# Kernel optimization log

Measured on AMD Instinct MI355X. Metric: run time of the kernel, lower is better.

Reference implementation:

```python
import jax, jax.numpy as jnp
import numpy as np

PRIMES = (2, 3, 5, 7, 11, 13, 17, 19, 23, 29)
TEMP = 1000.0  # softmax_temperature
B, S = 32, 2048

def _templates(p):
    # circle template for residue r: (cos(2*pi*r/p), sin(2*pi*r/p)) -> [p, 2]
    ang = 2.0 * np.pi * np.arange(p) / p
    return jnp.asarray(np.stack([np.cos(ang), np.sin(ang)], axis=-1).astype(np.float32))

def _mul_onehot(p):
    # onehot[a, b, (a*b) % p] = 1 -> [p, p, p]
    t = (np.arange(p)[:, None] * np.arange(p)[None, :]) % p
    return jnp.asarray((t[..., None] == np.arange(p)).astype(np.float32))

TEMPLATES = [_templates(p) for p in PRIMES]
MUL_OH = [_mul_onehot(p) for p in PRIMES]

def setup_inputs() -> dict:
    key = jax.random.key(0)
    k1, k2 = jax.random.split(key)
    m = len(PRIMES)
    return {
        "a_circle": jax.random.normal(k1, (B, S, m, 2), dtype=jnp.float32),
        "b_circle": jax.random.normal(k2, (B, S, m, 2), dtype=jnp.float32),
    }

def _circle_add(a, b):
    # complex multiply: angles add -> (a + b) mod p on the circle
    ca, sa = a[..., 0], a[..., 1]
    cb, sb = b[..., 0], b[..., 1]
    return jnp.stack([ca * cb - sa * sb, sa * cb + ca * sb], axis=-1)

def _circle_sub(a, b):
    # a - b = a + conj(b): negate sin of b
    b_conj = jnp.stack([b[..., 0], -b[..., 1]], axis=-1)
    return _circle_add(a, b_conj)

def _decode_soft(c_i, tmpl):
    # c_i: [B, S, 2], tmpl: [p, 2] -> soft one-hot over residues [B, S, p]
    sim = jnp.einsum('bsd,pd->bsp', c_i, tmpl)
    return jax.nn.softmax(TEMP * sim, axis=-1)

def _circle_mul(a, b):
    outs = []
    for i, p in enumerate(PRIMES):
        tmpl = TEMPLATES[i]
        a_soft = _decode_soft(a[:, :, i, :], tmpl)
        b_soft = _decode_soft(b[:, :, i, :], tmpl)
        # outer product of soft residues contracted with mul table
        dist = jnp.einsum('bsi,bsj,ijk->bsk', a_soft, b_soft, MUL_OH[i])
        outs.append(dist @ tmpl)  # re-encode to circle: [B, S, 2]
    return jnp.stack(outs, axis=2)  # [B, S, m, 2]

def reference(a_circle, b_circle):
    add = _circle_add(a_circle, b_circle)
    sub = _circle_sub(a_circle, b_circle)
    mul = _circle_mul(a_circle, b_circle)
    return jnp.stack([add, sub, mul], axis=0)  # [3, B, S, m, 2]
```

## Files before the change

### kernel.cpp

```cpp
#include <hip/hip_runtime.h>


#define SOFTMAX_TEMP 1000.0f

constexpr double PI_D = 3.14159265358979323846264338327950288;

constexpr double tay_cos(double x) {
    double x2 = x * x, term = 1.0, sum = 1.0;
    for (int k = 1; k <= 15; ++k) { term *= -x2 / double((2 * k - 1) * (2 * k)); sum += term; }
    return sum;
}
constexpr double tay_sin(double x) {
    double x2 = x * x, term = x, sum = x;
    for (int k = 1; k <= 15; ++k) { term *= -x2 / double((2 * k) * (2 * k + 1)); sum += term; }
    return sum;
}

template <int P> struct Tab { float c[P]; float s[P]; };

template <int P>
constexpr Tab<P> make_tab() {
    Tab<P> t{};
    for (int r = 0; r < P; ++r) {
        double x = 2.0 * PI_D * double(r) / double(P);
        if (x > PI_D) x -= 2.0 * PI_D;
        t.c[r] = (float)tay_cos(x);
        t.s[r] = (float)tay_sin(x);
    }
    return t;
}

template <int P>
__device__ __forceinline__ void mul_prime(float ca, float sa, float cb, float sb,
                                          float& oc, float& os) {
    constexpr Tab<P> T = make_tab<P>();

    float ma = -1e30f, mb = -1e30f;
#pragma unroll
    for (int r = 0; r < P; ++r) {
        ma = fmaxf(ma, ca * T.c[r] + sa * T.s[r]);
        mb = fmaxf(mb, cb * T.c[r] + sb * T.s[r]);
    }

    float eb[P];
    float Sb = 0.f;
#pragma unroll
    for (int r = 0; r < P; ++r) {
        float x = __expf(SOFTMAX_TEMP * (cb * T.c[r] + sb * T.s[r] - mb));
        eb[r] = x; Sb += x;
    }

    float W[P];
#pragma unroll
    for (int k = 0; k < P; ++k) W[k] = 0.f;

    float Sa = 0.f, ea0 = 0.f;
#pragma unroll
    for (int i = 0; i < P; ++i) {
        float ea_i = __expf(SOFTMAX_TEMP * (ca * T.c[i] + sa * T.s[i] - ma));
        Sa += ea_i;
        if (i == 0) { ea0 = ea_i; }
        else {
#pragma unroll
            for (int j = 1; j < P; ++j) {
                const int k = (i * j) % P;
                W[k] = fmaf(ea_i, eb[j], W[k]);
            }
        }
    }
    W[0] += ea0 * Sb + eb[0] * (Sa - ea0);

    float accC = 0.f, accS = 0.f;
#pragma unroll
    for (int k = 0; k < P; ++k) {
        accC = fmaf(W[k], T.c[k], accC);
        accS = fmaf(W[k], T.s[k], accS);
    }
    const float inv = 1.0f / (Sa * Sb);
    oc = accC * inv;
    os = accS * inv;
}

__global__ __launch_bounds__(256) void arith_kernel(const float* __restrict__ a,
                                                    const float* __restrict__ b,
                                                    float* __restrict__ out,
                                                    int n_pairs, int n_units) {
    const int lane = threadIdx.x & 63;
    const int unit = blockIdx.x * 4 + (threadIdx.x >> 6);
    if (unit >= n_units) return;
    const int pg = unit / 10;
    const int pi = unit - pg * 10;
    const int pair = pg * 64 + lane;
    if (pair >= n_pairs) return;

    const int base = pair * 20 + pi * 2;
    const float2 av = *(const float2*)(a + base);
    const float2 bv = *(const float2*)(b + base);
    const float ca = av.x, sa = av.y, cb = bv.x, sb = bv.y;

    const float pcc = ca * cb, pss = sa * sb, psc = sa * cb, pcs = ca * sb;
    const int plane = n_pairs * 20;
    *(float2*)(out + base)         = make_float2(pcc - pss, psc + pcs);
    *(float2*)(out + plane + base) = make_float2(pcc + pss, psc - pcs);

    float oc, os;
    switch (pi) {
        case 0: mul_prime<2>(ca, sa, cb, sb, oc, os); break;
        case 1: mul_prime<3>(ca, sa, cb, sb, oc, os); break;
        case 2: mul_prime<5>(ca, sa, cb, sb, oc, os); break;
        case 3: mul_prime<7>(ca, sa, cb, sb, oc, os); break;
        case 4: mul_prime<11>(ca, sa, cb, sb, oc, os); break;
        case 5: mul_prime<13>(ca, sa, cb, sb, oc, os); break;
        case 6: mul_prime<17>(ca, sa, cb, sb, oc, os); break;
        case 7: mul_prime<19>(ca, sa, cb, sb, oc, os); break;
        case 8: mul_prime<23>(ca, sa, cb, sb, oc, os); break;
        default: mul_prime<29>(ca, sa, cb, sb, oc, os); break;
    }
    *(float2*)(out + 2 * plane + base) = make_float2(oc, os);
}

extern "C" void kernel_launch(void* const* d_in, const int* in_sizes, int n_in,
                              void* d_out, int out_size, void* d_ws, size_t ws_size,
                              hipStream_t stream) {
    const float* a = (const float*)d_in[0];
    const float* b = (const float*)d_in[1];
    float* out = (float*)d_out;
    const int n_pairs = in_sizes[0] / 20;
    const int n_groups = (n_pairs + 63) / 64;
    const int n_units = n_groups * 10;
    const int n_blocks = (n_units + 3) / 4;

    dim3 block(256);
    dim3 grid(n_blocks);
    arith_kernel<<<grid, block, 0, stream>>>(a, b, out, n_pairs, n_units);
}
```

Before: 79.04 us.

## Stage input and output through shared memory for coalesced global access

```diff
diff --git a/kernel.cpp b/kernel.cpp
--- a/kernel.cpp
+++ b/kernel.cpp
@@ -81,27 +81,34 @@
     os = accS * inv;
 }
 
-__global__ __launch_bounds__(256) void arith_kernel(const float* __restrict__ a,
-                                                    const float* __restrict__ b,
-                                                    float* __restrict__ out,
-                                                    int n_pairs, int n_units) {
-    const int lane = threadIdx.x & 63;
-    const int unit = blockIdx.x * 4 + (threadIdx.x >> 6);
-    if (unit >= n_units) return;
-    const int pg = unit / 10;
-    const int pi = unit - pg * 10;
-    const int pair = pg * 64 + lane;
-    if (pair >= n_pairs) return;
+__global__ __launch_bounds__(640, 5) void arith_kernel(const float* __restrict__ a,
+                                                       const float* __restrict__ b,
+                                                       float* __restrict__ out,
+                                                       int n_pairs) {
+    __shared__ float t0[64 * 21], t1[64 * 21], t2[64 * 21];
 
-    const int base = pair * 20 + pi * 2;
-    const float2 av = *(const float2*)(a + base);
-    const float2 bv = *(const float2*)(b + base);
-    const float ca = av.x, sa = av.y, cb = bv.x, sb = bv.y;
+    const int t = threadIdx.x;
+    const int gbase = blockIdx.x * 1280;
+
+    {
+        const int e = 2 * t;
+        const int pr = e / 20, off = e - pr * 20;
+        const int la = pr * 21 + off;
+        const float2 av = *(const float2*)(a + gbase + e);
+        const float2 bv = *(const float2*)(b + gbase + e);
+        t0[la] = av.x; t0[la + 1] = av.y;
+        t1[la] = bv.x; t1[la + 1] = bv.y;
+    }
+    __syncthreads();
+
+    const int lane = t & 63;
+    const int pi = t >> 6;
+    const int la = lane * 21 + pi * 2;
+    const float ca = t0[la], sa = t0[la + 1];
+    const float cb = t1[la], sb = t1[la + 1];
+    __syncthreads();
 
     const float pcc = ca * cb, pss = sa * sb, psc = sa * cb, pcs = ca * sb;
-    const int plane = n_pairs * 20;
-    *(float2*)(out + base)         = make_float2(pcc - pss, psc + pcs);
-    *(float2*)(out + plane + base) = make_float2(pcc + pss, psc - pcs);
 
     float oc, os;
     switch (pi) {
@@ -116,7 +123,21 @@
         case 8: mul_prime<23>(ca, sa, cb, sb, oc, os); break;
         default: mul_prime<29>(ca, sa, cb, sb, oc, os); break;
     }
-    *(float2*)(out + 2 * plane + base) = make_float2(oc, os);
+
+    t0[la] = pcc - pss; t0[la + 1] = psc + pcs;
+    t1[la] = pcc + pss; t1[la + 1] = psc - pcs;
+    t2[la] = oc;        t2[la + 1] = os;
+    __syncthreads();
+
+    {
+        const int e = 2 * t;
+        const int pr = e / 20, off = e - pr * 20;
+        const int ls = pr * 21 + off;
+        const int plane = n_pairs * 20;
+        *(float2*)(out + gbase + e)             = make_float2(t0[ls], t0[ls + 1]);
+        *(float2*)(out + plane + gbase + e)     = make_float2(t1[ls], t1[ls + 1]);
+        *(float2*)(out + 2 * plane + gbase + e) = make_float2(t2[ls], t2[ls + 1]);
+    }
 }
 
 extern "C" void kernel_launch(void* const* d_in, const int* in_sizes, int n_in,
@@ -126,11 +147,9 @@
     const float* b = (const float*)d_in[1];
     float* out = (float*)d_out;
     const int n_pairs = in_sizes[0] / 20;
-    const int n_groups = (n_pairs + 63) / 64;
-    const int n_units = n_groups * 10;
-    const int n_blocks = (n_units + 3) / 4;
+    const int n_groups = n_pairs / 64;
 
-    dim3 block(256);
-    dim3 grid(n_blocks);
-    arith_kernel<<<grid, block, 0, stream>>>(a, b, out, n_pairs, n_units);
+    dim3 block(640);
+    dim3 grid(n_groups);
+    arith_kernel<<<grid, block, 0, stream>>>(a, b, out, n_pairs);
 }
```

After: 85.42 us. +8.1%, slower.
